# Kernel tuning notes

Measured on AMD Instinct MI355X. Metric: run time of the kernel, lower is better.

## Reference

```python
import jax, jax.numpy as jnp
import numpy as np

F_NODES = 360        # nodes per graph == num_features (square connectome)
NUM_GRAPHS = 128
NUM_EDGES = 1_000_000
C = 128              # hidden_channels
NUM_LAYERS = 3
HIDDEN = 512
NUM_CLASSES = 2
EPS = 1e-5


def _bn(x, g, b):
    # BatchNorm1d in training mode: biased batch statistics over the batch dim.
    m = x.mean(axis=0)
    v = x.var(axis=0)
    return (x - m) * jax.lax.rsqrt(v + EPS) * g + b


def _gcn(x, W, b, src, dst):
    # GCNConv: x' = D^{-1/2} (A + I) D^{-1/2} (x W) + b
    N = x.shape[0]
    h = x @ W                                   # [N, C]
    loop = jnp.arange(N, dtype=src.dtype)
    src2 = jnp.concatenate([src, loop])
    dst2 = jnp.concatenate([dst, loop])
    deg = jax.ops.segment_sum(jnp.ones_like(dst2, dtype=h.dtype), dst2, num_segments=N)
    dinv = jnp.where(deg > 0, jax.lax.rsqrt(deg), 0.0)
    norm = dinv[src2] * dinv[dst2]              # [E+N]
    out = jax.ops.segment_sum(h[src2] * norm[:, None], dst2, num_segments=N)
    return out + b


def setup_inputs() -> dict:
    key = jax.random.key(0)
    ks = jax.random.split(key, 16)
    N = NUM_GRAPHS * F_NODES
    x = jax.random.normal(ks[0], (N, F_NODES), jnp.float32)
    # edges confined within each graph
    g = jax.random.randint(ks[1], (NUM_EDGES,), 0, NUM_GRAPHS)
    edge_src = g * F_NODES + jax.random.randint(ks[2], (NUM_EDGES,), 0, F_NODES)
    edge_dst = g * F_NODES + jax.random.randint(ks[3], (NUM_EDGES,), 0, F_NODES)
    batch = jnp.repeat(jnp.arange(NUM_GRAPHS), F_NODES)

    def lin(k, fi, fo):
        s = 1.0 / np.sqrt(fi)
        return jax.random.uniform(k, (fi, fo), jnp.float32, -s, s)

    input_dim = F_NODES * (F_NODES + 1) // 2    # 64980
    input_dim1 = input_dim + C * NUM_LAYERS     # 65364
    H2 = HIDDEN // 2
    params = dict(
        Wc1=lin(ks[4], F_NODES, C), bc1=jnp.zeros((C,), jnp.float32),
        Wc2=lin(ks[5], C, C), bc2=jnp.zeros((C,), jnp.float32),
        Wc3=lin(ks[6], C, C), bc3=jnp.zeros((C,), jnp.float32),
        bn_g=jnp.ones((input_dim,), jnp.float32), bn_b=jnp.zeros((input_dim,), jnp.float32),
        bnh_g=jnp.ones((C * NUM_LAYERS,), jnp.float32), bnh_b=jnp.zeros((C * NUM_LAYERS,), jnp.float32),
        W1=lin(ks[7], input_dim1, HIDDEN), b1=jnp.zeros((HIDDEN,), jnp.float32),
        g1=jnp.ones((HIDDEN,), jnp.float32), be1=jnp.zeros((HIDDEN,), jnp.float32),
        W2=lin(ks[8], HIDDEN, H2), b2=jnp.zeros((H2,), jnp.float32),
        g2=jnp.ones((H2,), jnp.float32), be2=jnp.zeros((H2,), jnp.float32),
        W3=lin(ks[9], H2, H2), b3=jnp.zeros((H2,), jnp.float32),
        g3=jnp.ones((H2,), jnp.float32), be3=jnp.zeros((H2,), jnp.float32),
        W4=lin(ks[10], H2, NUM_CLASSES), b4=jnp.zeros((NUM_CLASSES,), jnp.float32),
    )
    return {"x": x, "edge_src": edge_src, "edge_dst": edge_dst, "batch": batch, **params}


def reference(x, edge_src, edge_dst, batch,
              Wc1, bc1, Wc2, bc2, Wc3, bc3,
              bn_g, bn_b, bnh_g, bnh_b,
              W1, b1, g1, be1, W2, b2, g2, be2, W3, b3, g3, be3, W4, b4):
    N, F = x.shape
    B = N // F                                   # nodes per graph == F
    # stacked GCN convs with tanh
    xs = [x]
    for W, b in ((Wc1, bc1), (Wc2, bc2), (Wc3, bc3)):
        xs.append(jnp.tanh(_gcn(xs[-1], W, b, edge_src, edge_dst)))
    # per-graph upper-triangular gather of the raw connectome (vectorized)
    iu0, iu1 = np.triu_indices(F)
    x0 = xs[0].reshape(B, F, F)[:, iu0, iu1]     # [B, F(F+1)/2]
    x0 = _bn(x0, bn_g, bn_b)
    # per-layer segment-mean pooling over graphs
    cnt = jax.ops.segment_sum(jnp.ones((N,), x.dtype), batch, num_segments=B)
    h = jnp.concatenate(
        [jax.ops.segment_sum(xx, batch, num_segments=B) / cnt[:, None] for xx in xs[1:]],
        axis=1)                                  # [B, C*num_layers]
    h = _bn(h, bnh_g, bnh_b)
    z = jnp.concatenate([x0, h], axis=1)         # [B, input_dim1]
    # MLP head (dropout in eval mode => identity)
    z = jax.nn.relu(_bn(z @ W1 + b1, g1, be1))
    z = jax.nn.relu(_bn(z @ W2 + b2, g2, be2))
    z = jax.nn.relu(_bn(z @ W3 + b3, g3, be3))
    return jax.nn.log_softmax(z @ W4 + b4, axis=1)
```

## Files before the change

kernel.cpp:

```cpp
#include <hip/hip_runtime.h>
#include <hip/hip_bf16.h>
#include <math.h>

#define FN 360
#define NG 128
#define NN 46080
#define CH 128
#define NE 1000000
#define TRI 64980
#define D1 65364
#define ZLD 65376
#define H1 512
#define H2 256
#define EPS 1e-5f
#define NSPLIT 64
#define NB1 720
#define ERNG 8192
#define NR 123
#define NCH 8
#define CROWS 45
#define BCAP 16
#define OVCAP 192
#define OVGCAP 32768
#define NAGG 384

typedef unsigned short u16;
typedef __attribute__((ext_vector_type(8))) short bf16x8;
typedef __attribute__((ext_vector_type(4))) float f32x4;

__device__ __forceinline__ float bf2f(u16 v) {
  union { unsigned u; float f; } x; x.u = ((unsigned)v) << 16; return x.f;
}
__device__ __forceinline__ u16 f2bf(float f) {
  union { float f; unsigned u; } x; x.f = f;
  unsigned r = x.u + 0x7fffu + ((x.u >> 16) & 1u);
  return (u16)(r >> 16);
}
__device__ __forceinline__ bf16x8 bzero8() {
  bf16x8 z;
#pragma unroll
  for (int j = 0; j < 8; j++) z[j] = 0;
  return z;
}

static const size_t Z_OFF    = 0;
static const size_t PART_OFF = 16736256;
static const size_t EBUF_OFF = PART_OFF;
static const size_t CNT_OFF  = PART_OFF + 4027392;
static const size_t OVF_OFF  = CNT_OFF + 503808;
static const size_t Y1_OFF   = 50290688;
static const size_t A1_OFF   = 50552832;
static const size_t A2_OFF   = 50683904;
static const size_t A3_OFF   = 50749440;
static const size_t DEG_OFF  = 66355200;
static const size_t HP_OFF   = 66539520;
static const size_t OVN_OFF  = 66736128;
static const size_t AB_OFF   = 66740224;
static const size_t PT_OFF   = 99917824;
static const size_t H_OFF    = 111714304;

__global__ __launch_bounds__(256) void k_gemm1deg(
    const float* __restrict__ X, const float* __restrict__ W,
    u16* __restrict__ PT,
    const int* __restrict__ src, const int* __restrict__ dst,
    float* __restrict__ deg, u16* __restrict__ ebuf, int* __restrict__ cnt,
    int* __restrict__ govn, unsigned* __restrict__ govf) {
  if (blockIdx.x >= NB1) {
    __shared__ int cur[NG * NCH];
    __shared__ u16 bins[NG * NCH][BCAP];
    __shared__ unsigned ovf[OVCAP];
    __shared__ int ovn, obase;
    int r = blockIdx.x - NB1;
    for (int i = threadIdx.x; i < NG * NCH; i += 256) cur[i] = 0;
    if (threadIdx.x == 0) ovn = 0;
    __syncthreads();
    int base = r * ERNG;
#pragma unroll 4
    for (int it = 0; it < ERNG / 256; it++) {
      int e = base + it * 256 + threadIdx.x;
      if (e < NE) {
        int s = src[e], d = dst[e];
        atomicAdd(&deg[d], 1.0f);
        int g = d / FN;
        int ls = s - g * FN, ld = d - g * FN;
        int ch = ld / CROWS;
        int gc = g * NCH + ch;
        int slot = atomicAdd(&cur[gc], 1);
        if (slot < BCAP) {
          bins[gc][slot] = (u16)(ls | ((ld - ch * CROWS) << 9));
        } else {
          int o = atomicAdd(&ovn, 1);
          if (o < OVCAP) ovf[o] = (unsigned)ls | ((unsigned)ld << 9) | ((unsigned)g << 18);
        }
      }
    }
    __syncthreads();
    {
      const f32x4* sb = (const f32x4*)bins;
      f32x4* gb = (f32x4*)(ebuf + (size_t)r * (NG * NCH) * BCAP);
      for (int i = threadIdx.x; i < NG * NCH * BCAP / 8; i += 256) gb[i] = sb[i];
    }
    for (int i = threadIdx.x; i < NG * NCH; i += 256) {
      int c = cur[i];
      cnt[r * (NG * NCH) + i] = c < BCAP ? c : BCAP;
    }
    if (threadIdx.x == 0) {
      int n = ovn < OVCAP ? ovn : OVCAP;
      obase = atomicAdd(govn, n);
    }
    __syncthreads();
    int n = ovn < OVCAP ? ovn : OVCAP;
    for (int i = threadIdx.x; i < n; i += 256)
      if (obase + i < OVGCAP) govf[obase + i] = ovf[i];
    return;
  }
  __shared__ __attribute__((aligned(16))) u16 WT[128][40];
  const int K = FN;
  int wid = threadIdx.x >> 6, lane = threadIdx.x & 63;
  int quad = lane >> 4, l16 = lane & 15;
  int m0 = blockIdx.x * 64 + (wid & 1) * 32;
  int n0w = (wid >> 1) * 64;
  int kl = threadIdx.x >> 3, nseg = (threadIdx.x & 7) * 16;
  f32x4 acc[2][4];
#pragma unroll
  for (int i = 0; i < 2; i++)
#pragma unroll
    for (int j = 0; j < 4; j++) acc[i][j] = (f32x4){0,0,0,0};
  for (int k0 = 0; k0 < K; k0 += 32) {
    __syncthreads();
    int kg = k0 + kl;
    if (kg < K) {
      const float* wrow = W + (size_t)kg * CH + nseg;
      f32x4 w0 = *(const f32x4*)(wrow);
      f32x4 w1 = *(const f32x4*)(wrow + 4);
      f32x4 w2 = *(const f32x4*)(wrow + 8);
      f32x4 w3 = *(const f32x4*)(wrow + 12);
#pragma unroll
      for (int j = 0; j < 4; j++) {
        WT[nseg + j][kl]      = f2bf(w0[j]);
        WT[nseg + 4 + j][kl]  = f2bf(w1[j]);
        WT[nseg + 8 + j][kl]  = f2bf(w2[j]);
        WT[nseg + 12 + j][kl] = f2bf(w3[j]);
      }
    } else {
#pragma unroll
      for (int j = 0; j < 16; j++) WT[nseg + j][kl] = 0;
    }
    __syncthreads();
    int kk = k0 + quad * 8;
    bool kin = kk < K;
    bf16x8 af[2];
#pragma unroll
    for (int tm = 0; tm < 2; tm++) {
      int row = m0 + tm * 16 + l16;
      bf16x8 a = bzero8();
      if (kin) {
        f32x4 va = *(const f32x4*)(X + (size_t)row * K + kk);
        f32x4 vb = *(const f32x4*)(X + (size_t)row * K + kk + 4);
#pragma unroll
        for (int j = 0; j < 4; j++) { a[j] = (short)f2bf(va[j]); a[4 + j] = (short)f2bf(vb[j]); }
      }
      af[tm] = a;
    }
    bf16x8 bfr[4];
#pragma unroll
    for (int tn = 0; tn < 4; tn++)
      bfr[tn] = *(const bf16x8*)&WT[n0w + tn * 16 + l16][quad * 8];
#pragma unroll
    for (int tm = 0; tm < 2; tm++)
#pragma unroll
      for (int tn = 0; tn < 4; tn++)
        acc[tm][tn] = __builtin_amdgcn_mfma_f32_16x16x32_bf16(af[tm], bfr[tn], acc[tm][tn], 0, 0, 0);
  }
#pragma unroll
  for (int tm = 0; tm < 2; tm++)
#pragma unroll
    for (int tn = 0; tn < 4; tn++) {
      int col = n0w + tn * 16 + l16;
      int rowb = m0 + tm * 16 + quad * 4;
#pragma unroll
      for (int r = 0; r < 4; r++) {
        int row = rowb + r;
        int g = row / FN, lr = row - g * FN;
        PT[((size_t)g * CH + col) * FN + lr] = f2bf(acc[tm][tn][r]);
      }
    }
}

__global__ __launch_bounds__(256) void k_abuild3(
    const u16* __restrict__ ebuf, const int* __restrict__ cnt,
    const int* __restrict__ govn, const unsigned* __restrict__ govf,
    const float* __restrict__ deg, u16* __restrict__ Ab) {
  __shared__ __attribute__((aligned(16))) float sA[CROWS * FN];
  __shared__ float sdg[FN];
  __shared__ int scnt[NR];
  int g = blockIdx.x >> 3, ch = blockIdx.x & 7;
  int gc = g * NCH + ch;
  int r0 = ch * CROWS;
  for (int i = threadIdx.x; i < CROWS * FN / 4; i += 256) ((f32x4*)sA)[i] = (f32x4){0,0,0,0};
  for (int i = threadIdx.x; i < FN; i += 256) sdg[i] = rsqrtf(deg[g * FN + i] + 1.0f);
  for (int i = threadIdx.x; i < NR; i += 256) scnt[i] = cnt[i * (NG * NCH) + gc];
  __syncthreads();
  for (int idx = threadIdx.x; idx < NR * BCAP; idx += 256) {
    int r = idx >> 4, sl = idx & (BCAP - 1);
    if (sl < scnt[r]) {
      u16 p = ebuf[((size_t)r * (NG * NCH) + gc) * BCAP + sl];
      int ls = p & 511, ldr = (p >> 9) & 63;
      atomicAdd(&sA[ldr * FN + ls], sdg[ls] * sdg[r0 + ldr]);
    }
  }
  int on = *govn; if (on > OVGCAP) on = OVGCAP;
  for (int i = threadIdx.x; i < on; i += 256) {
    unsigned p = govf[i];
    if ((int)(p >> 18) == g) {
      int ld = (p >> 9) & 511, lr = ld - r0;
      if ((unsigned)lr < (unsigned)CROWS) {
        int ls = p & 511;
        atomicAdd(&sA[lr * FN + ls], sdg[ls] * sdg[ld]);
      }
    }
  }
  __syncthreads();
  if (threadIdx.x < CROWS) {
    int l = r0 + threadIdx.x;
    float dv = sdg[l];
    sA[threadIdx.x * FN + l] += dv * dv;
  }
  __syncthreads();
  unsigned* dstu = (unsigned*)(Ab + (size_t)g * FN * FN + (size_t)r0 * FN);
  for (int i = threadIdx.x; i < CROWS * FN / 2; i += 256) {
    unsigned lo = f2bf(sA[2 * i]), hi = f2bf(sA[2 * i + 1]);
    dstu[i] = lo | (hi << 16);
  }
}

template<bool GUARD>
__device__ __forceinline__ void gbig_body(
    const u16* __restrict__ Z, const float* __restrict__ W1f,
    float* __restrict__ part, int s, int n0b) {
  __shared__ __attribute__((aligned(16))) u16 WT[128][40];
  int wid = threadIdx.x >> 6, lane = threadIdx.x & 63;
  int quad = lane >> 4, l16 = lane & 15;
  int m0 = wid * 32;
  int kl = threadIdx.x >> 3, nseg = (threadIdx.x & 7) * 16;
  int kbeg = s * 1024;
  int kend = GUARD ? ((ZLD < kbeg + 1024) ? ZLD : (kbeg + 1024)) : (kbeg + 1024);
  f32x4 acc[2][8];
#pragma unroll
  for (int i = 0; i < 2; i++)
#pragma unroll
    for (int j = 0; j < 8; j++) acc[i][j] = (f32x4){0,0,0,0};
  for (int k0 = kbeg; k0 < kend; k0 += 32) {
    __syncthreads();
    int kg = k0 + kl;
    if (!GUARD || kg < D1) {
      const float* wrow = W1f + (size_t)kg * H1 + n0b + nseg;
      f32x4 w0 = *(const f32x4*)(wrow);
      f32x4 w1 = *(const f32x4*)(wrow + 4);
      f32x4 w2 = *(const f32x4*)(wrow + 8);
      f32x4 w3 = *(const f32x4*)(wrow + 12);
#pragma unroll
      for (int j = 0; j < 4; j++) {
        WT[nseg + j][kl]      = f2bf(w0[j]);
        WT[nseg + 4 + j][kl]  = f2bf(w1[j]);
        WT[nseg + 8 + j][kl]  = f2bf(w2[j]);
        WT[nseg + 12 + j][kl] = f2bf(w3[j]);
      }
    } else {
#pragma unroll
      for (int j = 0; j < 16; j++) WT[nseg + j][kl] = 0;
    }
    __syncthreads();
    int kk = k0 + quad * 8;
    bf16x8 af[2];
#pragma unroll
    for (int tm = 0; tm < 2; tm++) {
      int row = m0 + tm * 16 + l16;
      af[tm] = *(const bf16x8*)(Z + (size_t)row * ZLD + kk);
    }
    bf16x8 bfr[8];
#pragma unroll
    for (int tn = 0; tn < 8; tn++)
      bfr[tn] = *(const bf16x8*)&WT[tn * 16 + l16][quad * 8];
#pragma unroll
    for (int tm = 0; tm < 2; tm++)
#pragma unroll
      for (int tn = 0; tn < 8; tn++)
        acc[tm][tn] = __builtin_amdgcn_mfma_f32_16x16x32_bf16(af[tm], bfr[tn], acc[tm][tn], 0, 0, 0);
  }
#pragma unroll
  for (int tm = 0; tm < 2; tm++)
#pragma unroll
    for (int tn = 0; tn < 8; tn++) {
      int col = n0b + tn * 16 + l16;
      int rowb = m0 + tm * 16 + quad * 4;
#pragma unroll
      for (int r = 0; r < 4; r++)
        part[((size_t)s * NG + rowb + r) * H1 + col] = acc[tm][tn][r];
    }
}

__global__ __launch_bounds__(256) void k_agg(
    const u16* __restrict__ Ab, const u16* __restrict__ PT,
    const float* __restrict__ bias, u16* __restrict__ Hout,
    float* __restrict__ hp, int loff,
    const u16* __restrict__ Z, const float* __restrict__ W1f,
    float* __restrict__ part) {
  if (blockIdx.x >= NAGG) {
    int id2 = blockIdx.x - NAGG;
    gbig_body<false>(Z, W1f, part, id2 >> 2, (id2 & 3) * 128);
    return;
  }
  __shared__ __attribute__((aligned(16))) u16 sA[128][40];
  __shared__ __attribute__((aligned(16))) u16 sP[128][40];
  __shared__ float ps[8][128];
  int id = blockIdx.x;
  int g = (id & 7) + 8 * (id / 24);
  int mb = (id % 24) >> 3;
  int m0blk = mb * 128;
  int wid = threadIdx.x >> 6, lane = threadIdx.x & 63;
  int quad = lane >> 4, l16 = lane & 15;
  int mw = (wid & 1) * 64, nw = (wid >> 1) * 64;
  const u16* Abg = Ab + (size_t)g * FN * FN;
  const u16* PTg = PT + (size_t)g * CH * FN;
  int t = threadIdx.x;
  f32x4 acc[4][4];
#pragma unroll
  for (int i = 0; i < 4; i++)
#pragma unroll
    for (int j = 0; j < 4; j++) acc[i][j] = (f32x4){0,0,0,0};
  bf16x8 ra[2], rp[2];
#define AGG_LOAD(k0)                                                          \
  {                                                                           \
    _Pragma("unroll")                                                         \
    for (int i = 0; i < 2; i++) {                                             \
      int lin = i * 256 + t;                                                  \
      int row = lin >> 2, q = lin & 3;                                        \
      int kg = (k0) + q * 8;                                                  \
      int grow = m0blk + row;                                                 \
      ra[i] = (kg < FN && grow < FN)                                          \
                  ? *(const bf16x8*)(Abg + (size_t)grow * FN + kg) : bzero8();\
      rp[i] = (kg < FN)                                                       \
                  ? *(const bf16x8*)(PTg + (size_t)row * FN + kg) : bzero8(); \
    }                                                                         \
  }
  AGG_LOAD(0)
  for (int step = 0; step < 12; step++) {
    __syncthreads();
#pragma unroll
    for (int i = 0; i < 2; i++) {
      int lin = i * 256 + t;
      int row = lin >> 2, q = lin & 3;
      *(bf16x8*)&sA[row][q * 8] = ra[i];
      *(bf16x8*)&sP[row][q * 8] = rp[i];
    }
    __syncthreads();
    if (step < 11) AGG_LOAD((step + 1) * 32)
    bf16x8 af[4], bp[4];
#pragma unroll
    for (int tm = 0; tm < 4; tm++)
      af[tm] = *(const bf16x8*)&sA[mw + tm * 16 + l16][quad * 8];
#pragma unroll
    for (int tn = 0; tn < 4; tn++)
      bp[tn] = *(const bf16x8*)&sP[nw + tn * 16 + l16][quad * 8];
#pragma unroll
    for (int tm = 0; tm < 4; tm++)
#pragma unroll
      for (int tn = 0; tn < 4; tn++)
        acc[tm][tn] = __builtin_amdgcn_mfma_f32_16x16x32_bf16(af[tm], bp[tn], acc[tm][tn], 0, 0, 0);
  }
#undef AGG_LOAD
  float lsum[4] = {0.f, 0.f, 0.f, 0.f};
#pragma unroll
  for (int tm = 0; tm < 4; tm++)
#pragma unroll
    for (int tn = 0; tn < 4; tn++) {
      int col = nw + tn * 16 + l16;
      float bc = bias[col];
      int rowb = m0blk + mw + tm * 16 + quad * 4;
#pragma unroll
      for (int r = 0; r < 4; r++) {
        int row = rowb + r;
        if (row < FN) {
          float tt = tanhf(acc[tm][tn][r] + bc);
          if (Hout) Hout[(size_t)(g * FN + row) * CH + col] = f2bf(tt);
          lsum[tn] += tt;
        }
      }
    }
  int cid = (wid & 1) * 4 + quad;
#pragma unroll
  for (int tn = 0; tn < 4; tn++) ps[cid][nw + tn * 16 + l16] = lsum[tn];
  __syncthreads();
  if (threadIdx.x < 128) {
    float s = 0.f;
#pragma unroll
    for (int c = 0; c < 8; c++) s += ps[c][threadIdx.x];
    atomicAdd(&hp[g * 384 + loff + threadIdx.x], s);
  }
}

__global__ __launch_bounds__(256) void k_gemm_xw_bf16(
    const u16* __restrict__ X, const float* __restrict__ W,
    u16* __restrict__ PT) {
  __shared__ __attribute__((aligned(16))) u16 WT[128][40];
  int wid = threadIdx.x >> 6, lane = threadIdx.x & 63;
  int quad = lane >> 4, l16 = lane & 15;
  int m0 = blockIdx.x * 64 + (wid & 1) * 32;
  int n0w = (wid >> 1) * 64;
  int kl = threadIdx.x >> 3, nseg = (threadIdx.x & 7) * 16;
  f32x4 acc[2][4];
#pragma unroll
  for (int i = 0; i < 2; i++)
#pragma unroll
    for (int j = 0; j < 4; j++) acc[i][j] = (f32x4){0,0,0,0};
  for (int k0 = 0; k0 < CH; k0 += 32) {
    __syncthreads();
    int kg = k0 + kl;
    const float* wrow = W + (size_t)kg * CH + nseg;
    f32x4 w0 = *(const f32x4*)(wrow);
    f32x4 w1 = *(const f32x4*)(wrow + 4);
    f32x4 w2 = *(const f32x4*)(wrow + 8);
    f32x4 w3 = *(const f32x4*)(wrow + 12);
#pragma unroll
    for (int j = 0; j < 4; j++) {
      WT[nseg + j][kl]      = f2bf(w0[j]);
      WT[nseg + 4 + j][kl]  = f2bf(w1[j]);
      WT[nseg + 8 + j][kl]  = f2bf(w2[j]);
      WT[nseg + 12 + j][kl] = f2bf(w3[j]);
    }
    __syncthreads();
    int kk = k0 + quad * 8;
    bf16x8 af[2];
#pragma unroll
    for (int tm = 0; tm < 2; tm++) {
      int row = m0 + tm * 16 + l16;
      af[tm] = *(const bf16x8*)(X + (size_t)row * CH + kk);
    }
    bf16x8 bfr[4];
#pragma unroll
    for (int tn = 0; tn < 4; tn++)
      bfr[tn] = *(const bf16x8*)&WT[n0w + tn * 16 + l16][quad * 8];
#pragma unroll
    for (int tm = 0; tm < 2; tm++)
#pragma unroll
      for (int tn = 0; tn < 4; tn++)
        acc[tm][tn] = __builtin_amdgcn_mfma_f32_16x16x32_bf16(af[tm], bfr[tn], acc[tm][tn], 0, 0, 0);
  }
#pragma unroll
  for (int tm = 0; tm < 2; tm++)
#pragma unroll
    for (int tn = 0; tn < 4; tn++) {
      int col = n0w + tn * 16 + l16;
      int rowb = m0 + tm * 16 + quad * 4;
#pragma unroll
      for (int r = 0; r < 4; r++) {
        int row = rowb + r;
        int g = row / FN, lr = row - g * FN;
        PT[((size_t)g * CH + col) * FN + lr] = f2bf(acc[tm][tn][r]);
      }
    }
}

__global__ __launch_bounds__(256) void k_gemm2tri(
    const u16* __restrict__ X, const float* __restrict__ W,
    u16* __restrict__ PT,
    const float* __restrict__ x, const float* __restrict__ gam,
    const float* __restrict__ bet, u16* __restrict__ z) {
  if (blockIdx.x >= NB1) {
    int i = blockIdx.x - NB1;
    int off = i * FN - (i * (i - 1)) / 2;
    for (int j = i + (int)threadIdx.x; j < FN; j += 256) {
      float s = 0.f, ss = 0.f;
#pragma unroll 8
      for (int b = 0; b < NG; b++) {
        float v = x[(size_t)(b * FN + i) * FN + j];
        s += v; ss += v * v;
      }
      float mean = s * (1.0f / NG);
      float var = fmaxf(ss * (1.0f / NG) - mean * mean, 0.f);
      float rstd = rsqrtf(var + EPS);
      int f = off + (j - i);
      float ga = gam[f] * rstd;
      float bb = bet[f] - mean * ga;
#pragma unroll 8
      for (int b = 0; b < NG; b++) {
        float v = x[(size_t)(b * FN + i) * FN + j];
        z[(size_t)b * ZLD + f] = f2bf(v * ga + bb);
      }
    }
    return;
  }
  __shared__ __attribute__((aligned(16))) u16 WT[128][40];
  int wid = threadIdx.x >> 6, lane = threadIdx.x & 63;
  int quad = lane >> 4, l16 = lane & 15;
  int m0 = blockIdx.x * 64 + (wid & 1) * 32;
  int n0w = (wid >> 1) * 64;
  int kl = threadIdx.x >> 3, nseg = (threadIdx.x & 7) * 16;
  f32x4 acc[2][4];
#pragma unroll
  for (int i = 0; i < 2; i++)
#pragma unroll
    for (int j = 0; j < 4; j++) acc[i][j] = (f32x4){0,0,0,0};
  for (int k0 = 0; k0 < CH; k0 += 32) {
    __syncthreads();
    int kg = k0 + kl;
    const float* wrow = W + (size_t)kg * CH + nseg;
    f32x4 w0 = *(const f32x4*)(wrow);
    f32x4 w1 = *(const f32x4*)(wrow + 4);
    f32x4 w2 = *(const f32x4*)(wrow + 8);
    f32x4 w3 = *(const f32x4*)(wrow + 12);
#pragma unroll
    for (int j = 0; j < 4; j++) {
      WT[nseg + j][kl]      = f2bf(w0[j]);
      WT[nseg + 4 + j][kl]  = f2bf(w1[j]);
      WT[nseg + 8 + j][kl]  = f2bf(w2[j]);
      WT[nseg + 12 + j][kl] = f2bf(w3[j]);
    }
    __syncthreads();
    int kk = k0 + quad * 8;
    bf16x8 af[2];
#pragma unroll
    for (int tm = 0; tm < 2; tm++) {
      int row = m0 + tm * 16 + l16;
      af[tm] = *(const bf16x8*)(X + (size_t)row * CH + kk);
    }
    bf16x8 bfr[4];
#pragma unroll
    for (int tn = 0; tn < 4; tn++)
      bfr[tn] = *(const bf16x8*)&WT[n0w + tn * 16 + l16][quad * 8];
#pragma unroll
    for (int tm = 0; tm < 2; tm++)
#pragma unroll
      for (int tn = 0; tn < 4; tn++)
        acc[tm][tn] = __builtin_amdgcn_mfma_f32_16x16x32_bf16(af[tm], bfr[tn], acc[tm][tn], 0, 0, 0);
  }
#pragma unroll
  for (int tm = 0; tm < 2; tm++)
#pragma unroll
    for (int tn = 0; tn < 4; tn++) {
      int col = n0w + tn * 16 + l16;
      int rowb = m0 + tm * 16 + quad * 4;
#pragma unroll
      for (int r = 0; r < 4; r++) {
        int row = rowb + r;
        int g = row / FN, lr = row - g * FN;
        PT[((size_t)g * CH + col) * FN + lr] = f2bf(acc[tm][tn][r]);
      }
    }
}

__global__ void k_hpbn(const float* __restrict__ hp,
                       const float* __restrict__ hgam, const float* __restrict__ hbet,
                       u16* __restrict__ z) {
  for (int c = threadIdx.x; c < 384; c += 256) {
    float s = 0.f, ss = 0.f;
#pragma unroll 8
    for (int m = 0; m < NG; m++) {
      float v = hp[m * 384 + c] * (1.0f / FN);
      s += v; ss += v * v;
    }
    float mean = s * (1.0f / NG);
    float var = fmaxf(ss * (1.0f / NG) - mean * mean, 0.f);
    float rstd = rsqrtf(var + EPS);
    float ga = hgam[c] * rstd;
    float bb = hbet[c] - mean * ga;
#pragma unroll 8
    for (int m = 0; m < NG; m++)
      z[(size_t)m * ZLD + TRI + c] = f2bf(hp[m * 384 + c] * (1.0f / FN) * ga + bb);
  }
  if (threadIdx.x < NG) {
    for (int t = 0; t < ZLD - D1; t++)
      z[(size_t)threadIdx.x * ZLD + D1 + t] = 0;
  }
}

__global__ __launch_bounds__(256) void k_gbig_tail(
    const u16* __restrict__ Z, const float* __restrict__ W1f, float* __restrict__ part) {
  gbig_body<true>(Z, W1f, part, NSPLIT - 1, blockIdx.x * 128);
}

__global__ void k_red(const float* __restrict__ part, float* __restrict__ y1) {
  int idx = blockIdx.x * 256 + threadIdx.x;
  float s = 0.f;
#pragma unroll 8
  for (int i = 0; i < NSPLIT; i++) s += part[(size_t)i * 65536 + idx];
  y1[idx] = s;
}

__global__ __launch_bounds__(256) void k_bnrelu(
    const float* __restrict__ y, const float* __restrict__ gam,
    const float* __restrict__ bet, u16* __restrict__ a, int N) {
  __shared__ float sb[4][64], sb2[4][64];
  int c63 = threadIdx.x & 63;
  int grp = threadIdx.x >> 6;
  int c = blockIdx.x * 64 + c63;
  float s = 0.f, ss = 0.f;
#pragma unroll 8
  for (int m = grp * 32; m < grp * 32 + 32; m++) {
    float v = y[(size_t)m * N + c]; s += v; ss += v * v;
  }
  sb[grp][c63] = s; sb2[grp][c63] = ss;
  __syncthreads();
  float S = sb[0][c63] + sb[1][c63] + sb[2][c63] + sb[3][c63];
  float SS = sb2[0][c63] + sb2[1][c63] + sb2[2][c63] + sb2[3][c63];
  float mean = S * (1.0f / NG);
  float var = fmaxf(SS * (1.0f / NG) - mean * mean, 0.f);
  float rstd = rsqrtf(var + EPS);
  float ga = gam[c] * rstd;
  float bb = bet[c] - mean * ga;
#pragma unroll 8
  for (int m = grp * 32; m < grp * 32 + 32; m++) {
    float v = y[(size_t)m * N + c] * ga + bb;
    a[(size_t)m * N + c] = f2bf(fmaxf(v, 0.f));
  }
}

__global__ __launch_bounds__(256) void k_mlpbn(
    const u16* __restrict__ A, const float* __restrict__ W,
    const float* __restrict__ gam, const float* __restrict__ bet,
    u16* __restrict__ aout, int K, int N) {
  __shared__ __attribute__((aligned(16))) u16 WT[64][40];
  __shared__ float rs[4][4][4][16], rss[4][4][4][16];
  int wid = threadIdx.x >> 6, lane = threadIdx.x & 63;
  int quad = lane >> 4, l16 = lane & 15;
  int n0b = blockIdx.x * 64;
  int m0 = wid * 32;
  int kl = threadIdx.x >> 3;
  int nseg = (threadIdx.x & 7) * 8;
  f32x4 acc[2][4];
#pragma unroll
  for (int i = 0; i < 2; i++)
#pragma unroll
    for (int j = 0; j < 4; j++) acc[i][j] = (f32x4){0,0,0,0};
  for (int k0 = 0; k0 < K; k0 += 32) {
    __syncthreads();
    const float* wrow = W + (size_t)(k0 + kl) * N + n0b + nseg;
    f32x4 w0 = *(const f32x4*)(wrow);
    f32x4 w1 = *(const f32x4*)(wrow + 4);
#pragma unroll
    for (int j = 0; j < 4; j++) {
      WT[nseg + j][kl]     = f2bf(w0[j]);
      WT[nseg + 4 + j][kl] = f2bf(w1[j]);
    }
    __syncthreads();
    int kk = k0 + quad * 8;
    bf16x8 af[2];
#pragma unroll
    for (int tm = 0; tm < 2; tm++) {
      int row = m0 + tm * 16 + l16;
      af[tm] = *(const bf16x8*)(A + (size_t)row * K + kk);
    }
    bf16x8 bfr[4];
#pragma unroll
    for (int tn = 0; tn < 4; tn++)
      bfr[tn] = *(const bf16x8*)&WT[tn * 16 + l16][quad * 8];
#pragma unroll
    for (int tm = 0; tm < 2; tm++)
#pragma unroll
      for (int tn = 0; tn < 4; tn++)
        acc[tm][tn] = __builtin_amdgcn_mfma_f32_16x16x32_bf16(af[tm], bfr[tn], acc[tm][tn], 0, 0, 0);
  }
  __syncthreads();
#pragma unroll
  for (int tn = 0; tn < 4; tn++) {
    float s = 0.f, ss = 0.f;
#pragma unroll
    for (int tm = 0; tm < 2; tm++)
#pragma unroll
      for (int r = 0; r < 4; r++) { float v = acc[tm][tn][r]; s += v; ss += v * v; }
    rs[wid][quad][tn][l16] = s;
    rss[wid][quad][tn][l16] = ss;
  }
  __syncthreads();
#pragma unroll
  for (int tn = 0; tn < 4; tn++) {
    float S = 0.f, SS = 0.f;
#pragma unroll
    for (int w = 0; w < 4; w++)
#pragma unroll
      for (int q = 0; q < 4; q++) { S += rs[w][q][tn][l16]; SS += rss[w][q][tn][l16]; }
    float mean = S * (1.0f / NG);
    float var = fmaxf(SS * (1.0f / NG) - mean * mean, 0.f);
    float rstd = rsqrtf(var + EPS);
    int col = n0b + tn * 16 + l16;
    float ga = gam[col] * rstd;
    float bb = bet[col] - mean * ga;
#pragma unroll
    for (int tm = 0; tm < 2; tm++) {
      int rowb = m0 + tm * 16 + quad * 4;
#pragma unroll
      for (int r = 0; r < 4; r++) {
        float v = acc[tm][tn][r] * ga + bb;
        aout[(size_t)(rowb + r) * N + col] = f2bf(fmaxf(v, 0.f));
      }
    }
  }
}

__global__ void k_head(const u16* __restrict__ a3, const float* __restrict__ W4,
                       const float* __restrict__ b4, float* __restrict__ out) {
  __shared__ float w4s[H2 * 2];
  int m = threadIdx.x;
  for (int i = m; i < H2 * 2; i += 128) w4s[i] = W4[i];
  __syncthreads();
  float a0 = b4[0], a1 = b4[1];
  for (int k0 = 0; k0 < H2; k0 += 8) {
    bf16x8 v = *(const bf16x8*)(a3 + (size_t)m * H2 + k0);
#pragma unroll
    for (int j = 0; j < 8; j++) {
      float f = bf2f((u16)v[j]);
      a0 += f * w4s[(k0 + j) * 2];
      a1 += f * w4s[(k0 + j) * 2 + 1];
    }
  }
  float mx = fmaxf(a0, a1);
  float lse = mx + logf(expf(a0 - mx) + expf(a1 - mx));
  out[m * 2]     = a0 - lse;
  out[m * 2 + 1] = a1 - lse;
}

extern "C" void kernel_launch(void* const* d_in, const int* in_sizes, int n_in,
                              void* d_out, int out_size, void* d_ws, size_t ws_size,
                              hipStream_t stream) {
  const float* x    = (const float*)d_in[0];
  const int* esrc   = (const int*)d_in[1];
  const int* edst   = (const int*)d_in[2];
  const float* Wc1 = (const float*)d_in[4];  const float* bc1 = (const float*)d_in[5];
  const float* Wc2 = (const float*)d_in[6];  const float* bc2 = (const float*)d_in[7];
  const float* Wc3 = (const float*)d_in[8];  const float* bc3 = (const float*)d_in[9];
  const float* bn_g = (const float*)d_in[10]; const float* bn_b = (const float*)d_in[11];
  const float* bnh_g = (const float*)d_in[12]; const float* bnh_b = (const float*)d_in[13];
  const float* W1 = (const float*)d_in[14];
  const float* g1 = (const float*)d_in[16]; const float* be1 = (const float*)d_in[17];
  const float* W2 = (const float*)d_in[18];
  const float* g2 = (const float*)d_in[20]; const float* be2 = (const float*)d_in[21];
  const float* W3 = (const float*)d_in[22];
  const float* g3 = (const float*)d_in[24]; const float* be3 = (const float*)d_in[25];
  const float* W4 = (const float*)d_in[26]; const float* b4 = (const float*)d_in[27];

  char* ws = (char*)d_ws;
  float* deg  = (float*)(ws + DEG_OFF);
  float* hp   = (float*)(ws + HP_OFF);
  int*   govn = (int*)(ws + OVN_OFF);
  u16*   Ab   = (u16*)(ws + AB_OFF);
  u16*   ebuf = (u16*)(ws + EBUF_OFF);
  int*   cnt  = (int*)(ws + CNT_OFF);
  unsigned* govf = (unsigned*)(ws + OVF_OFF);
  u16*   PT   = (u16*)(ws + PT_OFF);
  u16*   h    = (u16*)(ws + H_OFF);
  u16*   z    = (u16*)(ws + Z_OFF);
  float* part = (float*)(ws + PART_OFF);
  float* y1   = (float*)(ws + Y1_OFF);
  u16*   a1   = (u16*)(ws + A1_OFF);
  u16*   a2   = (u16*)(ws + A2_OFF);
  u16*   a3   = (u16*)(ws + A3_OFF);

  (void)hipMemsetAsync(deg, 0, (size_t)NN * 4 + (size_t)NG * 384 * 4 + 4, stream);

  dim3 b256(256);
  k_gemm1deg<<<dim3(NB1 + NR), b256, 0, stream>>>(x, Wc1, PT, esrc, edst, deg, ebuf, cnt, govn, govf);
  k_abuild3<<<dim3(NG * NCH), b256, 0, stream>>>(ebuf, cnt, govn, govf, deg, Ab);
  k_agg<<<dim3(NAGG), b256, 0, stream>>>(Ab, PT, bc1, h, hp, 0, z, W1, part);
  k_gemm2tri<<<dim3(NB1 + FN), b256, 0, stream>>>(h, Wc2, PT, x, bn_g, bn_b, z);
  k_agg<<<dim3(NAGG + 252), b256, 0, stream>>>(Ab, PT, bc2, h, hp, CH, z, W1, part);
  k_gemm_xw_bf16<<<dim3(NB1), b256, 0, stream>>>(h, Wc3, PT);
  k_agg<<<dim3(NAGG), b256, 0, stream>>>(Ab, PT, bc3, (u16*)nullptr, hp, 2 * CH, z, W1, part);
  k_hpbn<<<dim3(1), b256, 0, stream>>>(hp, bnh_g, bnh_b, z);
  k_gbig_tail<<<dim3(4), b256, 0, stream>>>(z, W1, part);
  k_red<<<dim3(65536 / 256), b256, 0, stream>>>(part, y1);
  k_bnrelu<<<dim3(H1 / 64), b256, 0, stream>>>(y1, g1, be1, a1, H1);
  k_mlpbn<<<dim3(H2 / 64), b256, 0, stream>>>(a1, W2, g2, be2, a2, H1, H2);
  k_mlpbn<<<dim3(H2 / 64), b256, 0, stream>>>(a2, W3, g3, be3, a3, H2, H2);
  k_head<<<dim3(1), dim3(128), 0, stream>>>(a3, W4, b4, (float*)d_out);
}
```

Baseline: 617.2 us.

## Coalesce transposed GEMM epilogue via LDS and split edge bucketing kernel

The three X·W GEMM kernels now stage the bf16 output tile in shared memory (reusing the weight tile storage through a union) and write transposed PT rows as 16-byte vectors, replacing scattered 2-byte stores. Edge bucketing is split out of the first GEMM into its own kernel. It now runs with smaller edge ranges per block (more blocks) and halved bin capacity, with workspace offsets and the abuild indexing adjusted to match. The aim is better store coalescing and more parallelism in bucketing. The cost is an extra launch, an extra barrier, and more overflow edges going through the global overflow list.

```diff
diff --git a/kernel.cpp b/kernel.cpp
--- a/kernel.cpp
+++ b/kernel.cpp
@@ -15,11 +15,11 @@
 #define EPS 1e-5f
 #define NSPLIT 64
 #define NB1 720
-#define ERNG 8192
-#define NR 123
+#define ERNG 4096
+#define NR 245
 #define NCH 8
 #define CROWS 45
-#define BCAP 16
+#define BCAP 8
 #define OVCAP 192
 #define OVGCAP 32768
 #define NAGG 384
@@ -46,8 +46,8 @@
 static const size_t Z_OFF    = 0;
 static const size_t PART_OFF = 16736256;
 static const size_t EBUF_OFF = PART_OFF;
-static const size_t CNT_OFF  = PART_OFF + 4027392;
-static const size_t OVF_OFF  = CNT_OFF + 503808;
+static const size_t CNT_OFF  = PART_OFF + 4014080;
+static const size_t OVF_OFF  = CNT_OFF + 1003520;
 static const size_t Y1_OFF   = 50290688;
 static const size_t A1_OFF   = 50552832;
 static const size_t A2_OFF   = 50683904;
@@ -59,66 +59,93 @@
 static const size_t PT_OFF   = 99917824;
 static const size_t H_OFF    = 111714304;
 
-__global__ __launch_bounds__(256) void k_gemm1deg(
-    const float* __restrict__ X, const float* __restrict__ W,
-    u16* __restrict__ PT,
+__device__ __forceinline__ void pt_epilogue(
+    u16 (*PST)[72], const f32x4 (*acc)[4], u16* __restrict__ PT,
+    int m0blk, int wid, int quad, int l16) {
+  int n0w = (wid >> 1) * 64;
+  int mh = (wid & 1) * 32;
+#pragma unroll
+  for (int tm = 0; tm < 2; tm++)
+#pragma unroll
+    for (int tn = 0; tn < 4; tn++) {
+      int col = n0w + tn * 16 + l16;
+#pragma unroll
+      for (int r = 0; r < 4; r++)
+        PST[col][mh + tm * 16 + quad * 4 + r] = f2bf(acc[tm][tn][r]);
+    }
+  __syncthreads();
+  int t = threadIdx.x;
+  int col = t >> 1, seg = t & 1;
+#pragma unroll
+  for (int u = 0; u < 4; u++) {
+    int lrl = seg * 32 + u * 8;
+    int row = m0blk + lrl;
+    int g = row / FN, lr = row - g * FN;
+    *(bf16x8*)(PT + ((size_t)g * CH + col) * FN + lr) = *(const bf16x8*)&PST[col][lrl];
+  }
+}
+
+__global__ __launch_bounds__(256) void k_bucket(
     const int* __restrict__ src, const int* __restrict__ dst,
     float* __restrict__ deg, u16* __restrict__ ebuf, int* __restrict__ cnt,
     int* __restrict__ govn, unsigned* __restrict__ govf) {
-  if (blockIdx.x >= NB1) {
-    __shared__ int cur[NG * NCH];
-    __shared__ u16 bins[NG * NCH][BCAP];
-    __shared__ unsigned ovf[OVCAP];
-    __shared__ int ovn, obase;
-    int r = blockIdx.x - NB1;
-    for (int i = threadIdx.x; i < NG * NCH; i += 256) cur[i] = 0;
-    if (threadIdx.x == 0) ovn = 0;
-    __syncthreads();
-    int base = r * ERNG;
+  __shared__ int cur[NG * NCH];
+  __shared__ u16 bins[NG * NCH][BCAP];
+  __shared__ unsigned ovf[OVCAP];
+  __shared__ int ovn, obase;
+  int r = blockIdx.x;
+  for (int i = threadIdx.x; i < NG * NCH; i += 256) cur[i] = 0;
+  if (threadIdx.x == 0) ovn = 0;
+  __syncthreads();
+  int base = r * ERNG;
 #pragma unroll 4
-    for (int it = 0; it < ERNG / 256; it++) {
-      int e = base + it * 256 + threadIdx.x;
-      if (e < NE) {
-        int s = src[e], d = dst[e];
-        atomicAdd(&deg[d], 1.0f);
-        int g = d / FN;
-        int ls = s - g * FN, ld = d - g * FN;
-        int ch = ld / CROWS;
-        int gc = g * NCH + ch;
-        int slot = atomicAdd(&cur[gc], 1);
-        if (slot < BCAP) {
-          bins[gc][slot] = (u16)(ls | ((ld - ch * CROWS) << 9));
-        } else {
-          int o = atomicAdd(&ovn, 1);
-          if (o < OVCAP) ovf[o] = (unsigned)ls | ((unsigned)ld << 9) | ((unsigned)g << 18);
-        }
-      }
-    }
-    __syncthreads();
-    {
-      const f32x4* sb = (const f32x4*)bins;
-      f32x4* gb = (f32x4*)(ebuf + (size_t)r * (NG * NCH) * BCAP);
-      for (int i = threadIdx.x; i < NG * NCH * BCAP / 8; i += 256) gb[i] = sb[i];
-    }
-    for (int i = threadIdx.x; i < NG * NCH; i += 256) {
-      int c = cur[i];
-      cnt[r * (NG * NCH) + i] = c < BCAP ? c : BCAP;
-    }
-    if (threadIdx.x == 0) {
-      int n = ovn < OVCAP ? ovn : OVCAP;
-      obase = atomicAdd(govn, n);
-    }
-    __syncthreads();
+  for (int it = 0; it < ERNG / 256; it++) {
+    int e = base + it * 256 + threadIdx.x;
+    if (e < NE) {
+      int s = src[e], d = dst[e];
+      atomicAdd(&deg[d], 1.0f);
+      int g = d / FN;
+      int ls = s - g * FN, ld = d - g * FN;
+      int ch = ld / CROWS;
+      int gc = g * NCH + ch;
+      int slot = atomicAdd(&cur[gc], 1);
+      if (slot < BCAP) {
+        bins[gc][slot] = (u16)(ls | ((ld - ch * CROWS) << 9));
+      } else {
+        int o = atomicAdd(&ovn, 1);
+        if (o < OVCAP) ovf[o] = (unsigned)ls | ((unsigned)ld << 9) | ((unsigned)g << 18);
+      }
+    }
+  }
+  __syncthreads();
+  {
+    const f32x4* sb = (const f32x4*)bins;
+    f32x4* gb = (f32x4*)(ebuf + (size_t)r * (NG * NCH) * BCAP);
+    for (int i = threadIdx.x; i < NG * NCH * BCAP / 8; i += 256) gb[i] = sb[i];
+  }
+  for (int i = threadIdx.x; i < NG * NCH; i += 256) {
+    int c = cur[i];
+    cnt[r * (NG * NCH) + i] = c < BCAP ? c : BCAP;
+  }
+  if (threadIdx.x == 0) {
     int n = ovn < OVCAP ? ovn : OVCAP;
-    for (int i = threadIdx.x; i < n; i += 256)
-      if (obase + i < OVGCAP) govf[obase + i] = ovf[i];
-    return;
-  }
-  __shared__ __attribute__((aligned(16))) u16 WT[128][40];
+    obase = atomicAdd(govn, n);
+  }
+  __syncthreads();
+  int n = ovn < OVCAP ? ovn : OVCAP;
+  for (int i = threadIdx.x; i < n; i += 256)
+    if (obase + i < OVGCAP) govf[obase + i] = ovf[i];
+}
+
+__global__ __launch_bounds__(256) void k_gemm1(
+    const float* __restrict__ X, const float* __restrict__ W,
+    u16* __restrict__ PT) {
+  __shared__ __attribute__((aligned(16))) union { u16 WT[128][40]; u16 PST[128][72]; } sh;
   const int K = FN;
   int wid = threadIdx.x >> 6, lane = threadIdx.x & 63;
   int quad = lane >> 4, l16 = lane & 15;
-  int m0 = blockIdx.x * 64 + (wid & 1) * 32;
+  int m0blk = blockIdx.x * 64;
+  int m0 = m0blk + (wid & 1) * 32;
   int n0w = (wid >> 1) * 64;
   int kl = threadIdx.x >> 3, nseg = (threadIdx.x & 7) * 16;
   f32x4 acc[2][4];
@@ -137,14 +164,14 @@
       f32x4 w3 = *(const f32x4*)(wrow + 12);
 #pragma unroll
       for (int j = 0; j < 4; j++) {
-        WT[nseg + j][kl]      = f2bf(w0[j]);
-        WT[nseg + 4 + j][kl]  = f2bf(w1[j]);
-        WT[nseg + 8 + j][kl]  = f2bf(w2[j]);
-        WT[nseg + 12 + j][kl] = f2bf(w3[j]);
+        sh.WT[nseg + j][kl]      = f2bf(w0[j]);
+        sh.WT[nseg + 4 + j][kl]  = f2bf(w1[j]);
+        sh.WT[nseg + 8 + j][kl]  = f2bf(w2[j]);
+        sh.WT[nseg + 12 + j][kl] = f2bf(w3[j]);
       }
     } else {
 #pragma unroll
-      for (int j = 0; j < 16; j++) WT[nseg + j][kl] = 0;
+      for (int j = 0; j < 16; j++) sh.WT[nseg + j][kl] = 0;
     }
     __syncthreads();
     int kk = k0 + quad * 8;
@@ -165,26 +192,15 @@
     bf16x8 bfr[4];
 #pragma unroll
     for (int tn = 0; tn < 4; tn++)
-      bfr[tn] = *(const bf16x8*)&WT[n0w + tn * 16 + l16][quad * 8];
+      bfr[tn] = *(const bf16x8*)&sh.WT[n0w + tn * 16 + l16][quad * 8];
 #pragma unroll
     for (int tm = 0; tm < 2; tm++)
 #pragma unroll
       for (int tn = 0; tn < 4; tn++)
         acc[tm][tn] = __builtin_amdgcn_mfma_f32_16x16x32_bf16(af[tm], bfr[tn], acc[tm][tn], 0, 0, 0);
   }
-#pragma unroll
-  for (int tm = 0; tm < 2; tm++)
-#pragma unroll
-    for (int tn = 0; tn < 4; tn++) {
-      int col = n0w + tn * 16 + l16;
-      int rowb = m0 + tm * 16 + quad * 4;
-#pragma unroll
-      for (int r = 0; r < 4; r++) {
-        int row = rowb + r;
-        int g = row / FN, lr = row - g * FN;
-        PT[((size_t)g * CH + col) * FN + lr] = f2bf(acc[tm][tn][r]);
-      }
-    }
+  __syncthreads();
+  pt_epilogue(sh.PST, acc, PT, m0blk, wid, quad, l16);
 }
 
 __global__ __launch_bounds__(256) void k_abuild3(
@@ -202,7 +218,7 @@
   for (int i = threadIdx.x; i < NR; i += 256) scnt[i] = cnt[i * (NG * NCH) + gc];
   __syncthreads();
   for (int idx = threadIdx.x; idx < NR * BCAP; idx += 256) {
-    int r = idx >> 4, sl = idx & (BCAP - 1);
+    int r = idx >> 3, sl = idx & (BCAP - 1);
     if (sl < scnt[r]) {
       u16 p = ebuf[((size_t)r * (NG * NCH) + gc) * BCAP + sl];
       int ls = p & 511, ldr = (p >> 9) & 63;
@@ -403,10 +419,11 @@
 __global__ __launch_bounds__(256) void k_gemm_xw_bf16(
     const u16* __restrict__ X, const float* __restrict__ W,
     u16* __restrict__ PT) {
-  __shared__ __attribute__((aligned(16))) u16 WT[128][40];
+  __shared__ __attribute__((aligned(16))) union { u16 WT[128][40]; u16 PST[128][72]; } sh;
   int wid = threadIdx.x >> 6, lane = threadIdx.x & 63;
   int quad = lane >> 4, l16 = lane & 15;
-  int m0 = blockIdx.x * 64 + (wid & 1) * 32;
+  int m0blk = blockIdx.x * 64;
+  int m0 = m0blk + (wid & 1) * 32;
   int n0w = (wid >> 1) * 64;
   int kl = threadIdx.x >> 3, nseg = (threadIdx.x & 7) * 16;
   f32x4 acc[2][4];
@@ -424,10 +441,10 @@
     f32x4 w3 = *(const f32x4*)(wrow + 12);
 #pragma unroll
     for (int j = 0; j < 4; j++) {
-      WT[nseg + j][kl]      = f2bf(w0[j]);
-      WT[nseg + 4 + j][kl]  = f2bf(w1[j]);
-      WT[nseg + 8 + j][kl]  = f2bf(w2[j]);
-      WT[nseg + 12 + j][kl] = f2bf(w3[j]);
+      sh.WT[nseg + j][kl]      = f2bf(w0[j]);
+      sh.WT[nseg + 4 + j][kl]  = f2bf(w1[j]);
+      sh.WT[nseg + 8 + j][kl]  = f2bf(w2[j]);
+      sh.WT[nseg + 12 + j][kl] = f2bf(w3[j]);
     }
     __syncthreads();
     int kk = k0 + quad * 8;
@@ -440,26 +457,15 @@
     bf16x8 bfr[4];
 #pragma unroll
     for (int tn = 0; tn < 4; tn++)
-      bfr[tn] = *(const bf16x8*)&WT[n0w + tn * 16 + l16][quad * 8];
+      bfr[tn] = *(const bf16x8*)&sh.WT[n0w + tn * 16 + l16][quad * 8];
 #pragma unroll
     for (int tm = 0; tm < 2; tm++)
 #pragma unroll
       for (int tn = 0; tn < 4; tn++)
         acc[tm][tn] = __builtin_amdgcn_mfma_f32_16x16x32_bf16(af[tm], bfr[tn], acc[tm][tn], 0, 0, 0);
   }
-#pragma unroll
-  for (int tm = 0; tm < 2; tm++)
-#pragma unroll
-    for (int tn = 0; tn < 4; tn++) {
-      int col = n0w + tn * 16 + l16;
-      int rowb = m0 + tm * 16 + quad * 4;
-#pragma unroll
-      for (int r = 0; r < 4; r++) {
-        int row = rowb + r;
-        int g = row / FN, lr = row - g * FN;
-        PT[((size_t)g * CH + col) * FN + lr] = f2bf(acc[tm][tn][r]);
-      }
-    }
+  __syncthreads();
+  pt_epilogue(sh.PST, acc, PT, m0blk, wid, quad, l16);
 }
 
 __global__ __launch_bounds__(256) void k_gemm2tri(
@@ -491,10 +497,11 @@
     }
     return;
   }
-  __shared__ __attribute__((aligned(16))) u16 WT[128][40];
+  __shared__ __attribute__((aligned(16))) union { u16 WT[128][40]; u16 PST[128][72]; } sh;
   int wid = threadIdx.x >> 6, lane = threadIdx.x & 63;
   int quad = lane >> 4, l16 = lane & 15;
-  int m0 = blockIdx.x * 64 + (wid & 1) * 32;
+  int m0blk = blockIdx.x * 64;
+  int m0 = m0blk + (wid & 1) * 32;
   int n0w = (wid >> 1) * 64;
   int kl = threadIdx.x >> 3, nseg = (threadIdx.x & 7) * 16;
   f32x4 acc[2][4];
@@ -512,10 +519,10 @@
     f32x4 w3 = *(const f32x4*)(wrow + 12);
 #pragma unroll
     for (int j = 0; j < 4; j++) {
-      WT[nseg + j][kl]      = f2bf(w0[j]);
-      WT[nseg + 4 + j][kl]  = f2bf(w1[j]);
-      WT[nseg + 8 + j][kl]  = f2bf(w2[j]);
-      WT[nseg + 12 + j][kl] = f2bf(w3[j]);
+      sh.WT[nseg + j][kl]      = f2bf(w0[j]);
+      sh.WT[nseg + 4 + j][kl]  = f2bf(w1[j]);
+      sh.WT[nseg + 8 + j][kl]  = f2bf(w2[j]);
+      sh.WT[nseg + 12 + j][kl] = f2bf(w3[j]);
     }
     __syncthreads();
     int kk = k0 + quad * 8;
@@ -528,26 +535,15 @@
     bf16x8 bfr[4];
 #pragma unroll
     for (int tn = 0; tn < 4; tn++)
-      bfr[tn] = *(const bf16x8*)&WT[n0w + tn * 16 + l16][quad * 8];
+      bfr[tn] = *(const bf16x8*)&sh.WT[n0w + tn * 16 + l16][quad * 8];
 #pragma unroll
     for (int tm = 0; tm < 2; tm++)
 #pragma unroll
       for (int tn = 0; tn < 4; tn++)
         acc[tm][tn] = __builtin_amdgcn_mfma_f32_16x16x32_bf16(af[tm], bfr[tn], acc[tm][tn], 0, 0, 0);
   }
-#pragma unroll
-  for (int tm = 0; tm < 2; tm++)
-#pragma unroll
-    for (int tn = 0; tn < 4; tn++) {
-      int col = n0w + tn * 16 + l16;
-      int rowb = m0 + tm * 16 + quad * 4;
-#pragma unroll
-      for (int r = 0; r < 4; r++) {
-        int row = rowb + r;
-        int g = row / FN, lr = row - g * FN;
-        PT[((size_t)g * CH + col) * FN + lr] = f2bf(acc[tm][tn][r]);
-      }
-    }
+  __syncthreads();
+  pt_epilogue(sh.PST, acc, PT, m0blk, wid, quad, l16);
 }
 
 __global__ void k_hpbn(const float* __restrict__ hp,
@@ -759,7 +755,8 @@
   (void)hipMemsetAsync(deg, 0, (size_t)NN * 4 + (size_t)NG * 384 * 4 + 4, stream);
 
   dim3 b256(256);
-  k_gemm1deg<<<dim3(NB1 + NR), b256, 0, stream>>>(x, Wc1, PT, esrc, edst, deg, ebuf, cnt, govn, govf);
+  k_bucket<<<dim3(NR), b256, 0, stream>>>(esrc, edst, deg, ebuf, cnt, govn, govf);
+  k_gemm1<<<dim3(NB1), b256, 0, stream>>>(x, Wc1, PT);
   k_abuild3<<<dim3(NG * NCH), b256, 0, stream>>>(ebuf, cnt, govn, govf, deg, Ab);
   k_agg<<<dim3(NAGG), b256, 0, stream>>>(Ab, PT, bc1, h, hp, 0, z, W1, part);
   k_gemm2tri<<<dim3(NB1 + FN), b256, 0, stream>>>(h, Wc2, PT, x, bn_g, bn_b, z);
```

Result: slower. 644.2 us (+4.4%).
